# Performance work log

Hardware: AMD Instinct MI355X
Metric: run time of the kernel (lower is better)

The kernel has to match this reference:

```python
import jax, jax.numpy as jnp
import numpy as np


def setup_inputs() -> dict:
    key = jax.random.key(0)
    # batch x channels(u,v,w) x D x H x W periodic velocity field
    x = jax.random.normal(key, (2, 3, 256, 256, 256), dtype=jnp.float32)
    return {"x": x}


def reference(x):
    # Faithful translation of the depthwise Conv3d with fixed finite-difference
    # taps and circular padding, expressed as circular shifts (jnp.roll).
    # torch conv = cross-correlation, padding=1 circular, so for a tap at
    # kernel index 2 the output reads x[i+1], index 0 reads x[i-1].
    u = x[:, 0]  # diff along last axis (W):   k_x taps [1,1,0]=-1, [1,1,2]=+1
    v = x[:, 1]  # diff along axis -2 (H):     k_y taps [1,0,1]=-1, [1,2,1]=+1
    w = x[:, 2]  # DIAGONAL diff along (D,H):  k_z taps [0,0,1]=-1, [2,2,1]=+1
    du = jnp.roll(u, -1, axis=-1) - jnp.roll(u, 1, axis=-1)
    dv = jnp.roll(v, -1, axis=-2) - jnp.roll(v, 1, axis=-2)
    dw = jnp.roll(w, (-1, -1), axis=(-3, -2)) - jnp.roll(w, (1, 1), axis=(-3, -2))
    # sum over channels then * 0.5 (central-difference normalization)
    return 0.5 * (du + dv + dw)
```

## Files before the change

### kernel.cpp

```cpp
#include <hip/hip_runtime.h>


#define N     256
#define PLANE (N * N)
#define VOL   (N * N * N)

typedef float f4 __attribute__((ext_vector_type(4)));

__global__ __launch_bounds__(256)
void calc_divergence_4406636445920_kernel(const float* __restrict__ x,
                                          float* __restrict__ out) {
    const int tx = threadIdx.x;
    const int x0 = tx << 2;

    const int lin   = blockIdx.x;
    const int chunk = lin & 7;
    const int s     = lin >> 3;
    const int yblk  = s & 63;
    const int bz    = chunk * 64 + (s >> 6);
    const int z     = bz & (N - 1);
    const int b     = bz >> 8;
    const int y     = (yblk << 2) + threadIdx.y;

    const float* __restrict__ u = x + (size_t)(b * 3 + 0) * VOL;
    const float* __restrict__ v = x + (size_t)(b * 3 + 1) * VOL;
    const float* __restrict__ w = x + (size_t)(b * 3 + 2) * VOL;

    const int ym = (y == 0)     ? N - 1 : y - 1;
    const int yp = (y == N - 1) ? 0     : y + 1;
    const int zm = (z == 0)     ? N - 1 : z - 1;
    const int zp = (z == N - 1) ? 0     : z + 1;

    const int rowz = z * PLANE;
    const int rowc = rowz + y * N;

    const f4 uc = __builtin_nontemporal_load((const f4*)(u + rowc + x0));
    const float ul = __shfl(uc.w, (tx + 63) & 63);
    const float ur = __shfl(uc.x, (tx + 1)  & 63);

    const f4 vp = *(const f4*)(v + rowz + yp * N + x0);
    const f4 vm = *(const f4*)(v + rowz + ym * N + x0);
    const f4 wp = *(const f4*)(w + zp * PLANE + yp * N + x0);
    const f4 wm = *(const f4*)(w + zm * PLANE + ym * N + x0);

    f4 o;
    o.x = 0.5f * ((uc.y - ul)   + (vp.x - vm.x) + (wp.x - wm.x));
    o.y = 0.5f * ((uc.z - uc.x) + (vp.y - vm.y) + (wp.y - wm.y));
    o.z = 0.5f * ((uc.w - uc.y) + (vp.z - vm.z) + (wp.z - wm.z));
    o.w = 0.5f * ((ur   - uc.z) + (vp.w - vm.w) + (wp.w - wm.w));

    __builtin_nontemporal_store(o, (f4*)(out + (size_t)b * VOL + rowc + x0));
}

extern "C" void kernel_launch(void* const* d_in, const int* in_sizes, int n_in,
                              void* d_out, int out_size, void* d_ws, size_t ws_size,
                              hipStream_t stream) {
    const float* xin = (const float*)d_in[0];
    float* out = (float*)d_out;

    dim3 block(64, 4, 1);
    dim3 grid(2 * N * (N / 4), 1, 1);

    calc_divergence_4406636445920_kernel<<<grid, block, 0, stream>>>(xin, out);
}
```

Baseline: 548.9 us.

## Convert divergence kernel to persistent grid-stride loop with two rows per thread

Replaces the one-row-per-thread launch of 32768 blocks with a 1024-block persistent grid that loops over z planes, each thread processing two y rows per iteration with an unroll of 2. This amortizes block launch and index setup and increases memory-level parallelism per thread. The blocks-to-(batch, z range) mapping changes, which alters how the neighbouring w and v planes are shared in cache across concurrently running blocks. Fewer blocks may leave the memory system less saturated.

```diff
diff --git a/kernel.cpp b/kernel.cpp
--- a/kernel.cpp
+++ b/kernel.cpp
@@ -7,59 +7,92 @@
 
 typedef float f4 __attribute__((ext_vector_type(4)));
 
-__global__ __launch_bounds__(256)
+__global__ __launch_bounds__(256, 4)
 void calc_divergence_4406636445920_kernel(const float* __restrict__ x,
                                           float* __restrict__ out) {
     const int tx = threadIdx.x;
+    const int ty = threadIdx.y;
     const int x0 = tx << 2;
+    const int lm = (tx + 63) & 63;
+    const int lp = (tx + 1) & 63;
 
-    const int lin   = blockIdx.x;
-    const int chunk = lin & 7;
-    const int s     = lin >> 3;
-    const int yblk  = s & 63;
-    const int bz    = chunk * 64 + (s >> 6);
-    const int z     = bz & (N - 1);
-    const int b     = bz >> 8;
-    const int y     = (yblk << 2) + threadIdx.y;
+    const int chunk = blockIdx.x & 7;
+    const int cb    = blockIdx.x >> 3;
+
+    const int b     = chunk >> 2;
+    const int zbase = (chunk & 3) << 6;
 
     const float* __restrict__ u = x + (size_t)(b * 3 + 0) * VOL;
     const float* __restrict__ v = x + (size_t)(b * 3 + 1) * VOL;
     const float* __restrict__ w = x + (size_t)(b * 3 + 2) * VOL;
+    float* __restrict__ ob      = out + (size_t)b * VOL;
 
-    const int ym = (y == 0)     ? N - 1 : y - 1;
-    const int yp = (y == N - 1) ? 0     : y + 1;
-    const int zm = (z == 0)     ? N - 1 : z - 1;
-    const int zp = (z == N - 1) ? 0     : z + 1;
+    const int ypair = cb & 31;
+    const int yA  = ((ypair)      << 2) + ty;
+    const int yB  = ((ypair + 32) << 2) + ty;
+    const int yAm = (yA == 0)     ? N - 1 : yA - 1;
+    const int yAp = (yA == N - 1) ? 0     : yA + 1;
+    const int yBm = (yB == 0)     ? N - 1 : yB - 1;
+    const int yBp = (yB == N - 1) ? 0     : yB + 1;
 
-    const int rowz = z * PLANE;
-    const int rowc = rowz + y * N;
+    const int ryA  = yA  * N + x0;
+    const int ryAp = yAp * N + x0;
+    const int ryAm = yAm * N + x0;
+    const int ryB  = yB  * N + x0;
+    const int ryBp = yBp * N + x0;
+    const int ryBm = yBm * N + x0;
 
-    const f4 uc = __builtin_nontemporal_load((const f4*)(u + rowc + x0));
-    const float ul = __shfl(uc.w, (tx + 63) & 63);
-    const float ur = __shfl(uc.x, (tx + 1)  & 63);
+#pragma unroll 2
+    for (int p = cb; p < 2048; p += 128) {
+        const int zl = p >> 5;
+        const int z  = zbase + zl;
+        const int zm = (z == 0)     ? N - 1 : z - 1;
+        const int zp = (z == N - 1) ? 0     : z + 1;
 
-    const f4 vp = *(const f4*)(v + rowz + yp * N + x0);
-    const f4 vm = *(const f4*)(v + rowz + ym * N + x0);
-    const f4 wp = *(const f4*)(w + zp * PLANE + yp * N + x0);
-    const f4 wm = *(const f4*)(w + zm * PLANE + ym * N + x0);
+        const size_t rz  = (size_t)z  * PLANE;
+        const size_t rzp = (size_t)zp * PLANE;
+        const size_t rzm = (size_t)zm * PLANE;
 
-    f4 o;
-    o.x = 0.5f * ((uc.y - ul)   + (vp.x - vm.x) + (wp.x - wm.x));
-    o.y = 0.5f * ((uc.z - uc.x) + (vp.y - vm.y) + (wp.y - wm.y));
-    o.z = 0.5f * ((uc.w - uc.y) + (vp.z - vm.z) + (wp.z - wm.z));
-    o.w = 0.5f * ((ur   - uc.z) + (vp.w - vm.w) + (wp.w - wm.w));
+        const f4 uA  = __builtin_nontemporal_load((const f4*)(u + rz + ryA));
+        const f4 uB  = __builtin_nontemporal_load((const f4*)(u + rz + ryB));
+        const f4 vpA = *(const f4*)(v + rz + ryAp);
+        const f4 vmA = *(const f4*)(v + rz + ryAm);
+        const f4 vpB = *(const f4*)(v + rz + ryBp);
+        const f4 vmB = *(const f4*)(v + rz + ryBm);
+        const f4 wpA = *(const f4*)(w + rzp + ryAp);
+        const f4 wmA = *(const f4*)(w + rzm + ryAm);
+        const f4 wpB = *(const f4*)(w + rzp + ryBp);
+        const f4 wmB = *(const f4*)(w + rzm + ryBm);
 
-    __builtin_nontemporal_store(o, (f4*)(out + (size_t)b * VOL + rowc + x0));
+        const float ulA = __shfl(uA.w, lm);
+        const float urA = __shfl(uA.x, lp);
+        const float ulB = __shfl(uB.w, lm);
+        const float urB = __shfl(uB.x, lp);
+
+        f4 oA, oB;
+        oA.x = 0.5f * ((uA.y - ulA)  + (vpA.x - vmA.x) + (wpA.x - wmA.x));
+        oA.y = 0.5f * ((uA.z - uA.x) + (vpA.y - vmA.y) + (wpA.y - wmA.y));
+        oA.z = 0.5f * ((uA.w - uA.y) + (vpA.z - vmA.z) + (wpA.z - wmA.z));
+        oA.w = 0.5f * ((urA  - uA.z) + (vpA.w - vmA.w) + (wpA.w - wmA.w));
+
+        oB.x = 0.5f * ((uB.y - ulB)  + (vpB.x - vmB.x) + (wpB.x - wmB.x));
+        oB.y = 0.5f * ((uB.z - uB.x) + (vpB.y - vmB.y) + (wpB.y - wmB.y));
+        oB.z = 0.5f * ((uB.w - uB.y) + (vpB.z - vmB.z) + (wpB.z - wmB.z));
+        oB.w = 0.5f * ((urB  - uB.z) + (vpB.w - vmB.w) + (wpB.w - wmB.w));
+
+        __builtin_nontemporal_store(oA, (f4*)(ob + rz + ryA));
+        __builtin_nontemporal_store(oB, (f4*)(ob + rz + ryB));
+    }
 }
 
 extern "C" void kernel_launch(void* const* d_in, const int* in_sizes, int n_in,
                               void* d_out, int out_size, void* d_ws, size_t ws_size,
                               hipStream_t stream) {
     const float* xin = (const float*)d_in[0];
-    float* out = (float*)d_out;
+    float* o = (float*)d_out;
 
     dim3 block(64, 4, 1);
-    dim3 grid(2 * N * (N / 4), 1, 1);
+    dim3 grid(1024, 1, 1);
 
-    calc_divergence_4406636445920_kernel<<<grid, block, 0, stream>>>(xin, out);
+    calc_divergence_4406636445920_kernel<<<grid, block, 0, stream>>>(xin, o);
 }
```

Measured after the change: 558.5 us. About the same (+1.8%).
